# Optimization experiments

Measured on AMD Instinct MI355X. Metric: run time of the kernel, lower is better.

## Reference

```python
import jax, jax.numpy as jnp
import numpy as np

B, C, H, W, K = 4, 32, 64, 64, 64
BH, BW = 2, 2  # block_size
RF_THRESH = 0.05  # gaussian support threshold (lattice kernels are ~0 outside RF)


def _gaussian_lattice(key, n_kernels, h, w):
    """Build Gaussian receptive-field kernels like lattice.gaussian_kernel_lattice:
    rfs[k,i,j] = exp(-((i-mu_y)^2 + (j-mu_x)^2) / (2*sigma^2)), thresholded to
    zero outside the RF so each kernel has compact support."""
    k1, k2 = jax.random.split(key)
    mu = jax.random.uniform(k1, (n_kernels, 2), minval=8.0, maxval=h - 8.0)
    sigma = jax.random.uniform(k2, (n_kernels, 1), minval=4.0, maxval=7.0)
    yy = jnp.arange(h, dtype=jnp.float32)[:, None]
    xx = jnp.arange(w, dtype=jnp.float32)[None, :]
    d2 = (yy[None] - mu[:, 0, None, None]) ** 2 + (xx[None] - mu[:, 1, None, None]) ** 2
    g = jnp.exp(-d2 / (2.0 * sigma[:, :, None] ** 2))  # (K, h, w)
    return jnp.where(g > RF_THRESH, g, 0.0).astype(jnp.float32)


def setup_inputs() -> dict:
    key = jax.random.key(0)
    ku, kr = jax.random.split(key)
    u = jax.random.normal(ku, (B, C, H, W), dtype=jnp.float32)
    rfs = _gaussian_lattice(kr, K, H, W)
    return {"u": u, "rfs": rfs}


def reference(u, rfs):
    """RF_Pool.__call__ with pool_type='prob', block_size=(2,2): returns p_mean.

    For each receptive field k, the kernel is elementwise-multiplied with u and
    a probabilistic max-pool (Lee et al.) with an 'off' state is computed over
    the RF support:  h_mean_k = exp(u*rf_k) / (1 + sum_{RF_k} exp(u*rf_k)).
    Detection probabilities are accumulated over RFs, then pooling-unit means
    p_mean are taken as the block-wise max over block_size blocks."""
    dt = u.dtype
    mask = rfs > 0  # (K, H, W) RF supports
    neg = jnp.asarray(-1e30, dt)
    # kernel-weighted pre-activations per RF: (B, C, K, H, W)
    v = u[:, :, None, :, :] * rfs[None, None]
    vm = jnp.where(mask[None, None], v, neg)
    # stable normalization including the off-state exp(0)=1
    m = jnp.maximum(jnp.max(vm, axis=(-2, -1), keepdims=True), 0.0)
    e = jnp.where(mask[None, None], jnp.exp(v - m), 0.0)
    denom = jnp.exp(-m) + jnp.sum(e, axis=(-2, -1), keepdims=True)
    h_mean = jnp.sum(e / denom, axis=2)  # (B, C, H, W) sum over RFs
    # block-wise pooling to p_mean: (B, C, H//BH, W//BW)
    p_mean = h_mean.reshape(B, C, H // BH, BH, W // BW, BW).max(axis=(3, 5))
    return p_mean
```

## Files before the change

### kernel.cpp

```cpp
#include <hip/hip_runtime.h>
#include <hip/hip_bf16.h>

#define BB 4
#define CC 32
#define HH 64
#define WW 64
#define KK 64
#define PIX (HH * WW)
#define NBC (BB * CC)


__global__ __launch_bounds__(256) void rf_phase1(
        const float* __restrict__ u,
        const float* __restrict__ rfs,
        float* __restrict__ inv) {
    const int bc = blockIdx.x >> 4;
    const int kg = blockIdx.x & 15;
    const int t  = threadIdx.x;
    const int w  = t >> 6;
    const int l  = t & 63;

    __shared__ float su[PIX];
    {
        const float4* u4  = (const float4*)(u + (size_t)bc * PIX);
        float4*       su4 = (float4*)su;
        #pragma unroll
        for (int i = 0; i < 4; ++i) su4[t + 256 * i] = u4[t + 256 * i];
    }
    __syncthreads();

    const int k = kg * 4 + w;
    const float4* r4  = (const float4*)(rfs + (size_t)k * PIX);
    const float4* su4 = (const float4*)su;

    float s = 0.f;
    #pragma unroll
    for (int i = 0; i < 16; ++i) {
        const float4 rv = r4[64 * i + l];
        const float4 uv = su4[64 * i + l];
        const float ex = __expf(uv.x * rv.x);
        const float ey = __expf(uv.y * rv.y);
        const float ez = __expf(uv.z * rv.z);
        const float ew = __expf(uv.w * rv.w);
        s += (rv.x > 0.f) ? ex : 0.f;
        s += (rv.y > 0.f) ? ey : 0.f;
        s += (rv.z > 0.f) ? ez : 0.f;
        s += (rv.w > 0.f) ? ew : 0.f;
    }
    #pragma unroll
    for (int off = 32; off > 0; off >>= 1)
        s += __shfl_xor(s, off, 64);

    if (l == 0) inv[bc * KK + k] = 1.f / (1.f + s);
}

__global__ __launch_bounds__(256) void rf_phase2(
        const float* __restrict__ u,
        const float* __restrict__ rfs,
        const float* __restrict__ inv,
        float* __restrict__ out) {
    const int bc = blockIdx.x >> 3;
    const int rp = (blockIdx.x & 7) * 4 + (threadIdx.x >> 6);
    const int l  = threadIdx.x & 63;

    const int pbase = rp * 128 + l;
    const float u0 = u[(size_t)bc * PIX + pbase];
    const float u1 = u[(size_t)bc * PIX + pbase + 64];
    const float* __restrict__ invp = inv + bc * KK;
    const float* __restrict__ rfp  = rfs + pbase;

    float h0 = 0.f, h1 = 0.f;
    #pragma unroll 8
    for (int k = 0; k < KK; ++k) {
        const float r0 = rfp[(size_t)k * PIX];
        const float r1 = rfp[(size_t)k * PIX + 64];
        const float fi = invp[k];
        const float e0 = __expf(u0 * r0);
        const float e1 = __expf(u1 * r1);
        h0 += (r0 > 0.f) ? e0 * fi : 0.f;
        h1 += (r1 > 0.f) ? e1 * fi : 0.f;
    }

    const float v = fmaxf(h0, h1);
    const float o = fmaxf(v, __shfl_xor(v, 1, 64));
    if ((l & 1) == 0)
        out[(size_t)bc * (HH / 2) * (WW / 2) + rp * 32 + (l >> 1)] = o;
}

extern "C" void kernel_launch(void* const* d_in, const int* in_sizes, int n_in,
                              void* d_out, int out_size, void* d_ws, size_t ws_size,
                              hipStream_t stream) {
    const float* u   = (const float*)d_in[0];
    const float* rfs = (const float*)d_in[1];
    float* out       = (float*)d_out;
    float* inv       = (float*)d_ws;

    rf_phase1<<<NBC * 16, 256, 0, stream>>>(u, rfs, inv);
    rf_phase2<<<NBC * 8, 256, 0, stream>>>(u, rfs, inv, out);
}
```

Measured before the change: 73.30 us.

## Compact RF supports into sparse lists and iterate only nonzero entries

Adds a prep kernel that compacts each receptive field's nonzero pixels into a per-kernel list and builds, for each pixel, a list of the kernels covering it. Both phases then loop only over the sparse support, skipping the exp and masked work on zero RF entries. This runs every call, so it is not caching. The cost is an extra launch, indirect gathers of u, and variable-length loops that can diverge within a wavefront.

```diff
diff --git a/kernel.cpp b/kernel.cpp
--- a/kernel.cpp
+++ b/kernel.cpp
@@ -1,5 +1,4 @@
 #include <hip/hip_runtime.h>
-#include <hip/hip_bf16.h>
 
 #define BB 4
 #define CC 32
@@ -10,75 +9,125 @@
 #define NBC (BB * CC)
 
 
+#define OFF_INV    0
+#define OFF_KCNT   8192
+#define OFF_PCNT   8320
+#define OFF_PLIST  12416
+#define OFF_PXLIST 143488
+
+__global__ __launch_bounds__(256) void rf_prep(
+        const float* __restrict__ rfs, float* __restrict__ ws) {
+    int*    kcnt   = (int*)(ws + OFF_KCNT);
+    int*    pcnt   = (int*)(ws + OFF_PCNT);
+    float2* plist  = (float2*)(ws + OFF_PLIST);
+    float2* pxlist = (float2*)(ws + OFF_PXLIST);
+    const int bid = blockIdx.x;
+
+    if (bid < KK) {
+        const int k = bid;
+        const int t = threadIdx.x, w = t >> 6, l = t & 63;
+        __shared__ int scnt[4];
+        const float* rk = rfs + (size_t)k * PIX;
+        unsigned long long masks[16];
+        float vals[16];
+        int cnt = 0;
+        #pragma unroll
+        for (int i = 0; i < 16; ++i) {
+            const int p = (w * 16 + i) * 64 + l;
+            const float v = rk[p];
+            vals[i] = v;
+            const unsigned long long m = __ballot(v > 0.f);
+            masks[i] = m;
+            cnt += __popcll(m);
+        }
+        if (l == 0) scnt[w] = cnt;
+        __syncthreads();
+        int base = 0;
+        #pragma unroll
+        for (int j = 0; j < 4; ++j) base += (j < w) ? scnt[j] : 0;
+        if (w == 3 && l == 0) kcnt[k] = base + cnt;
+        const unsigned long long lmask = (1ull << l) - 1ull;
+        #pragma unroll
+        for (int i = 0; i < 16; ++i) {
+            const int p = (w * 16 + i) * 64 + l;
+            const unsigned long long m = masks[i];
+            if (vals[i] > 0.f) {
+                const int idx = base + (int)__popcll(m & lmask);
+                plist[k * 1024 + idx] = make_float2(vals[i], __int_as_float(p));
+            }
+            base += (int)__popcll(m);
+        }
+    } else {
+        const int p = (bid - KK) * 256 + threadIdx.x;
+        int c = 0;
+        for (int k = 0; k < KK; ++k) {
+            const float v = rfs[(size_t)k * PIX + p];
+            if (v > 0.f) {
+                pxlist[c * PIX + p] = make_float2(v, __int_as_float(k));
+                ++c;
+            }
+        }
+        pcnt[p] = c;
+    }
+}
+
 __global__ __launch_bounds__(256) void rf_phase1(
-        const float* __restrict__ u,
-        const float* __restrict__ rfs,
-        float* __restrict__ inv) {
+        const float* __restrict__ u, float* __restrict__ ws) {
+    float*        inv   = ws + OFF_INV;
+    const int*    kcnt  = (const int*)(ws + OFF_KCNT);
+    const float2* plist = (const float2*)(ws + OFF_PLIST);
+
     const int bc = blockIdx.x >> 4;
-    const int kg = blockIdx.x & 15;
-    const int t  = threadIdx.x;
-    const int w  = t >> 6;
-    const int l  = t & 63;
+    const int k  = (blockIdx.x & 15) * 4 + (threadIdx.x >> 6);
+    const int l  = threadIdx.x & 63;
 
-    __shared__ float su[PIX];
-    {
-        const float4* u4  = (const float4*)(u + (size_t)bc * PIX);
-        float4*       su4 = (float4*)su;
-        #pragma unroll
-        for (int i = 0; i < 4; ++i) su4[t + 256 * i] = u4[t + 256 * i];
-    }
-    __syncthreads();
-
-    const int k = kg * 4 + w;
-    const float4* r4  = (const float4*)(rfs + (size_t)k * PIX);
-    const float4* su4 = (const float4*)su;
+    const int n = kcnt[k];
+    const float*  up = u + (size_t)bc * PIX;
+    const float2* lp = plist + k * 1024;
 
     float s = 0.f;
-    #pragma unroll
-    for (int i = 0; i < 16; ++i) {
-        const float4 rv = r4[64 * i + l];
-        const float4 uv = su4[64 * i + l];
-        const float ex = __expf(uv.x * rv.x);
-        const float ey = __expf(uv.y * rv.y);
-        const float ez = __expf(uv.z * rv.z);
-        const float ew = __expf(uv.w * rv.w);
-        s += (rv.x > 0.f) ? ex : 0.f;
-        s += (rv.y > 0.f) ? ey : 0.f;
-        s += (rv.z > 0.f) ? ez : 0.f;
-        s += (rv.w > 0.f) ? ew : 0.f;
+    for (int e = l; e < n; e += 64) {
+        const float2 ev = lp[e];
+        const float uu  = up[__float_as_int(ev.y)];
+        s += __expf(uu * ev.x);
     }
     #pragma unroll
     for (int off = 32; off > 0; off >>= 1)
         s += __shfl_xor(s, off, 64);
-
     if (l == 0) inv[bc * KK + k] = 1.f / (1.f + s);
 }
 
 __global__ __launch_bounds__(256) void rf_phase2(
-        const float* __restrict__ u,
-        const float* __restrict__ rfs,
-        const float* __restrict__ inv,
+        const float* __restrict__ u, const float* __restrict__ ws,
         float* __restrict__ out) {
+    const float*  inv    = ws + OFF_INV;
+    const int*    pcnt   = (const int*)(ws + OFF_PCNT);
+    const float2* pxlist = (const float2*)(ws + OFF_PXLIST);
+
+    __shared__ float sld[KK];
     const int bc = blockIdx.x >> 3;
-    const int rp = (blockIdx.x & 7) * 4 + (threadIdx.x >> 6);
-    const int l  = threadIdx.x & 63;
+    const int t  = threadIdx.x;
+    if (t < KK) sld[t] = inv[bc * KK + t];
+    __syncthreads();
 
-    const int pbase = rp * 128 + l;
-    const float u0 = u[(size_t)bc * PIX + pbase];
-    const float u1 = u[(size_t)bc * PIX + pbase + 64];
-    const float* __restrict__ invp = inv + bc * KK;
-    const float* __restrict__ rfp  = rfs + pbase;
+    const int rp = (blockIdx.x & 7) * 4 + (t >> 6);
+    const int l  = t & 63;
+    const int p0 = rp * 128 + l;
+    const int p1 = p0 + 64;
+
+    const float u0 = u[(size_t)bc * PIX + p0];
+    const float u1 = u[(size_t)bc * PIX + p1];
+    const int   c0 = pcnt[p0];
+    const int   c1 = pcnt[p1];
 
     float h0 = 0.f, h1 = 0.f;
-    #pragma unroll 8
-    for (int k = 0; k < KK; ++k) {
-        const float r0 = rfp[(size_t)k * PIX];
-        const float r1 = rfp[(size_t)k * PIX + 64];
-        const float fi = invp[k];
-        const float e0 = __expf(u0 * r0);
-        const float e1 = __expf(u1 * r1);
-        h0 += (r0 > 0.f) ? e0 * fi : 0.f;
-        h1 += (r1 > 0.f) ? e1 * fi : 0.f;
+    for (int s = 0; s < c0; ++s) {
+        const float2 ev = pxlist[s * PIX + p0];
+        h0 += __expf(u0 * ev.x) * sld[__float_as_int(ev.y)];
+    }
+    for (int s = 0; s < c1; ++s) {
+        const float2 ev = pxlist[s * PIX + p1];
+        h1 += __expf(u1 * ev.x) * sld[__float_as_int(ev.y)];
     }
 
     const float v = fmaxf(h0, h1);
@@ -93,8 +142,9 @@
     const float* u   = (const float*)d_in[0];
     const float* rfs = (const float*)d_in[1];
     float* out       = (float*)d_out;
-    float* inv       = (float*)d_ws;
+    float* ws        = (float*)d_ws;
 
-    rf_phase1<<<NBC * 16, 256, 0, stream>>>(u, rfs, inv);
-    rf_phase2<<<NBC * 8, 256, 0, stream>>>(u, rfs, inv, out);
+    rf_prep  <<<KK + PIX / 256, 256, 0, stream>>>(rfs, ws);
+    rf_phase1<<<NBC * 16,       256, 0, stream>>>(u, ws);
+    rf_phase2<<<NBC * 8,        256, 0, stream>>>(u, ws, out);
 }
```

Measured after the change: 94.28 us. +28.6%, slower.

## Use raw exp2 with prescaled inputs and give each phase-2 thread a full 2x2 pool block

Applied to the files above, without the earlier changes.

Both kernels now prescale u by log2(e) and call the hardware exp2 builtin directly, which removes the multiply that __expf performs. Phase 2 is restructured so each thread computes a whole 2x2 pooling block with float2 loads of rfs, avoiding the cross-lane shuffle. The per-RF normalizers are staged in shared memory, and the grid is halved (4 blocks per batch-channel instead of 8). Fewer blocks and more work per thread may reduce occupancy and latency hiding, and the float2 rfs loads change the coalescing pattern.

```diff
diff --git a/kernel.cpp b/kernel.cpp
--- a/kernel.cpp
+++ b/kernel.cpp
@@ -1,5 +1,4 @@
 #include <hip/hip_runtime.h>
-#include <hip/hip_bf16.h>
 
 #define BB 4
 #define CC 32
@@ -8,6 +7,12 @@
 #define KK 64
 #define PIX (HH * WW)
 #define NBC (BB * CC)
+
+#define LOG2E 1.4426950408889634f
+
+static __device__ __forceinline__ float fexp2(float x) {
+    return __builtin_amdgcn_exp2f(x);
+}
 
 
 __global__ __launch_bounds__(256) void rf_phase1(
@@ -25,7 +30,11 @@
         const float4* u4  = (const float4*)(u + (size_t)bc * PIX);
         float4*       su4 = (float4*)su;
         #pragma unroll
-        for (int i = 0; i < 4; ++i) su4[t + 256 * i] = u4[t + 256 * i];
+        for (int i = 0; i < 4; ++i) {
+            float4 v = u4[t + 256 * i];
+            v.x *= LOG2E; v.y *= LOG2E; v.z *= LOG2E; v.w *= LOG2E;
+            su4[t + 256 * i] = v;
+        }
     }
     __syncthreads();
 
@@ -38,14 +47,10 @@
     for (int i = 0; i < 16; ++i) {
         const float4 rv = r4[64 * i + l];
         const float4 uv = su4[64 * i + l];
-        const float ex = __expf(uv.x * rv.x);
-        const float ey = __expf(uv.y * rv.y);
-        const float ez = __expf(uv.z * rv.z);
-        const float ew = __expf(uv.w * rv.w);
-        s += (rv.x > 0.f) ? ex : 0.f;
-        s += (rv.y > 0.f) ? ey : 0.f;
-        s += (rv.z > 0.f) ? ez : 0.f;
-        s += (rv.w > 0.f) ? ew : 0.f;
+        s += (rv.x > 0.f) ? fexp2(uv.x * rv.x) : 0.f;
+        s += (rv.y > 0.f) ? fexp2(uv.y * rv.y) : 0.f;
+        s += (rv.z > 0.f) ? fexp2(uv.z * rv.z) : 0.f;
+        s += (rv.w > 0.f) ? fexp2(uv.w * rv.w) : 0.f;
     }
     #pragma unroll
     for (int off = 32; off > 0; off >>= 1)
@@ -59,32 +64,41 @@
         const float* __restrict__ rfs,
         const float* __restrict__ inv,
         float* __restrict__ out) {
-    const int bc = blockIdx.x >> 3;
-    const int rp = (blockIdx.x & 7) * 4 + (threadIdx.x >> 6);
-    const int l  = threadIdx.x & 63;
+    __shared__ float sld[KK];
+    const int bc    = blockIdx.x >> 2;
+    const int strip = blockIdx.x & 3;
+    const int t     = threadIdx.x;
+    if (t < KK) sld[t] = inv[bc * KK + t];
+    __syncthreads();
 
-    const int pbase = rp * 128 + l;
-    const float u0 = u[(size_t)bc * PIX + pbase];
-    const float u1 = u[(size_t)bc * PIX + pbase + 64];
-    const float* __restrict__ invp = inv + bc * KK;
-    const float* __restrict__ rfp  = rfs + pbase;
+    const int qr = t >> 5;
+    const int qc = t & 31;
+    const int row0 = strip * 16 + 2 * qr;
+    const int p00  = row0 * 64 + 2 * qc;
+    const int p10  = p00 + 64;
 
-    float h0 = 0.f, h1 = 0.f;
-    #pragma unroll 8
+    const float* ub = u + (size_t)bc * PIX;
+    float2 ua = *(const float2*)(ub + p00);
+    float2 uc = *(const float2*)(ub + p10);
+    ua.x *= LOG2E; ua.y *= LOG2E; uc.x *= LOG2E; uc.y *= LOG2E;
+
+    const float* rp0 = rfs + p00;
+    const float* rp1 = rfs + p10;
+
+    float h00 = 0.f, h01 = 0.f, h10 = 0.f, h11 = 0.f;
+    #pragma unroll 4
     for (int k = 0; k < KK; ++k) {
-        const float r0 = rfp[(size_t)k * PIX];
-        const float r1 = rfp[(size_t)k * PIX + 64];
-        const float fi = invp[k];
-        const float e0 = __expf(u0 * r0);
-        const float e1 = __expf(u1 * r1);
-        h0 += (r0 > 0.f) ? e0 * fi : 0.f;
-        h1 += (r1 > 0.f) ? e1 * fi : 0.f;
+        const float2 ra = *(const float2*)(rp0 + (size_t)k * PIX);
+        const float2 rb = *(const float2*)(rp1 + (size_t)k * PIX);
+        const float  fi = sld[k];
+        h00 += ((ra.x > 0.f) ? fi : 0.f) * fexp2(ua.x * ra.x);
+        h01 += ((ra.y > 0.f) ? fi : 0.f) * fexp2(ua.y * ra.y);
+        h10 += ((rb.x > 0.f) ? fi : 0.f) * fexp2(uc.x * rb.x);
+        h11 += ((rb.y > 0.f) ? fi : 0.f) * fexp2(uc.y * rb.y);
     }
 
-    const float v = fmaxf(h0, h1);
-    const float o = fmaxf(v, __shfl_xor(v, 1, 64));
-    if ((l & 1) == 0)
-        out[(size_t)bc * (HH / 2) * (WW / 2) + rp * 32 + (l >> 1)] = o;
+    const float o = fmaxf(fmaxf(h00, h01), fmaxf(h10, h11));
+    out[(size_t)bc * (HH / 2) * (WW / 2) + (strip * 8 + qr) * 32 + qc] = o;
 }
 
 extern "C" void kernel_launch(void* const* d_in, const int* in_sizes, int n_in,
@@ -96,5 +110,5 @@
     float* inv       = (float*)d_ws;
 
     rf_phase1<<<NBC * 16, 256, 0, stream>>>(u, rfs, inv);
-    rf_phase2<<<NBC * 8, 256, 0, stream>>>(u, rfs, inv, out);
+    rf_phase2<<<NBC * 4,  256, 0, stream>>>(u, rfs, inv, out);
 }
```

Measured after the change: 82.18 us. 12.1% more time.
